# Kernel tuning notes

Measured on AMD Instinct MI355X. Metric: run time of the kernel, lower is better.

The kernel has to match this reference:

```python
import jax, jax.numpy as jnp
import numpy as np

TOP_K = 2
NUM_EXPERTS = 8

def setup_inputs() -> dict:
    key = jax.random.key(0)
    k_x, k_r, k_g, k_u, k_d = jax.random.split(key, 5)
    B, L, D, H, E = 1, 2048, 1024, 2048, NUM_EXPERTS
    scale = 0.02  # keep router logits / activations in a sane range
    return {
        "x": jax.random.normal(k_x, (B, L, D), dtype=jnp.float32),
        "router_w": jax.random.normal(k_r, (D, E), dtype=jnp.float32) * scale,
        "gate_w": jax.random.normal(k_g, (E, D, H), dtype=jnp.float32) * scale,
        "up_w": jax.random.normal(k_u, (E, D, H), dtype=jnp.float32) * scale,
        "down_w": jax.random.normal(k_d, (E, H, D), dtype=jnp.float32) * scale,
    }

def reference(x, router_w, gate_w, up_w, down_w):
    # x: (B, L, D)
    B, L, D = x.shape
    T = B * L
    E = router_w.shape[1]
    xf = x.reshape(T, D)

    # --- router: top-k softmax over selected logits (Mixtral-style) ---
    logits = xf @ router_w                      # (T, E)
    top_vals, top_idx = jax.lax.top_k(logits, TOP_K)  # (T, K)
    top_w = jax.nn.softmax(top_vals, axis=-1)   # (T, K)

    # combine weights scattered to dense (T, E); zeros for unrouted experts
    combine = jnp.zeros((T, E), dtype=x.dtype).at[
        jnp.arange(T)[:, None], top_idx
    ].add(top_w)

    # --- experts: SwiGLU, computed per expert, zero-weight tokens masked by combine ---
    gate = jnp.einsum('td,edh->eth', xf, gate_w)   # (E, T, H)
    up = jnp.einsum('td,edh->eth', xf, up_w)       # (E, T, H)
    hidden = jax.nn.silu(gate) * up                # (E, T, H)
    expert_out = jnp.einsum('eth,ehd->etd', hidden, down_w)  # (E, T, D)

    # --- weighted combine (equivalent to scatter_add over sorted assignments) ---
    y = jnp.einsum('etd,te->td', expert_out, combine)  # (T, D)
    return y.reshape(B, L, D)
```

## Files before the change

kernel.cpp:

```cpp
#include <hip/hip_runtime.h>
#include <hip/hip_bf16.h>
#include <stdint.h>

#define T_TOK 2048
#define DIM   1024
#define HDIM  2048
#define NE    8
#define ROWS_PAD 4224
#define TSLOTS 40

typedef __attribute__((ext_vector_type(8))) short bf16x8;
typedef __attribute__((ext_vector_type(4))) float f32x4;

__device__ __forceinline__ unsigned short f2bf(float f) {
    union { float f; unsigned int u; } v; v.f = f;
    unsigned int r = v.u + 0x7FFF + ((v.u >> 16) & 1);
    return (unsigned short)(r >> 16);
}

__device__ __forceinline__ float bf2f(unsigned short b) {
    union { unsigned int u; float f; } v; v.u = ((unsigned int)b) << 16;
    return v.f;
}

__device__ __forceinline__ void gload16(const void* g, void* l) {
    __builtin_amdgcn_global_load_lds(
        (const __attribute__((address_space(1))) void*)g,
        (__attribute__((address_space(3))) void*)l, 16, 0, 0);
}

#define NTT (3 * 16384)
__global__ void prep_kernel(const float* __restrict__ gw, const float* __restrict__ uw,
                            const float* __restrict__ dw,
                            unsigned short* __restrict__ WgT, unsigned short* __restrict__ WuT,
                            unsigned short* __restrict__ WdT,
                            const float* __restrict__ x, const float* __restrict__ rw,
                            int* __restrict__ counts, int* __restrict__ top_idx,
                            float* __restrict__ top_w) {
    __shared__ float tile[32][33];
    const int b = blockIdx.x;
    if (b < NTT) {
        const int m = b >> 14;
        const int t = b & 16383;
        const int e = t >> 11;
        const int rem = t & 2047;
        const float* in; unsigned short* out; int R, C, by, bx;
        if (m == 0)      { in = gw; out = WgT; R = DIM;  C = HDIM; by = rem >> 6; bx = rem & 63; }
        else if (m == 1) { in = uw; out = WuT; R = DIM;  C = HDIM; by = rem >> 6; bx = rem & 63; }
        else             { in = dw; out = WdT; R = HDIM; C = DIM;  by = rem >> 5; bx = rem & 31; }
        const float* ip = in + (size_t)e * R * C;
        unsigned short* op = out + (size_t)e * R * C;
        const int tx = threadIdx.x & 31, ty = threadIdx.x >> 5;
#pragma unroll
        for (int i = 0; i < 4; ++i)
            tile[ty + i * 8][tx] = ip[(size_t)(by * 32 + ty + i * 8) * C + bx * 32 + tx];
        __syncthreads();
#pragma unroll
        for (int i = 0; i < 2; ++i) {
            int oc = i * 16 + (threadIdx.x >> 4);
            int orw2 = (threadIdx.x & 15) * 2;
            ushort2 v;
            v.x = f2bf(tile[orw2][oc]);
            v.y = f2bf(tile[orw2 + 1][oc]);
            *(ushort2*)&op[(size_t)(bx * 32 + oc) * R + by * 32 + orw2] = v;
        }
    } else {
        const int wid = (b - NTT) * 4 + (threadIdx.x >> 6);
        const int lane = threadIdx.x & 63;
        if (wid >= T_TOK) return;
        float acc[NE];
#pragma unroll
        for (int e = 0; e < NE; ++e) acc[e] = 0.f;
        const float* xr = x + (size_t)wid * DIM;
        for (int i = lane; i < DIM; i += 64) {
            float xv = xr[i];
            const float* wr = rw + (size_t)i * NE;
#pragma unroll
            for (int e = 0; e < NE; ++e) acc[e] += xv * wr[e];
        }
#pragma unroll
        for (int off = 32; off; off >>= 1) {
#pragma unroll
            for (int e = 0; e < NE; ++e) acc[e] += __shfl_xor(acc[e], off, 64);
        }
        if (lane == 0) {
            float v0 = -1e30f, v1 = -1e30f; int i0 = 0, i1 = 0;
#pragma unroll
            for (int e = 0; e < NE; ++e) {
                float v = acc[e];
                if (v > v0) { v1 = v0; i1 = i0; v0 = v; i0 = e; }
                else if (v > v1) { v1 = v; i1 = e; }
            }
            float e1 = __expf(v1 - v0);
            float s = 1.f + e1;
            top_idx[wid * 2]     = i0;
            top_idx[wid * 2 + 1] = i1;
            top_w[wid * 2]     = 1.f / s;
            top_w[wid * 2 + 1] = e1 / s;
            atomicAdd(&counts[i0], 1);
            atomicAdd(&counts[i1], 1);
        }
    }
}

__global__ void scan_kernel(const int* __restrict__ counts, int* __restrict__ offsets,
                            int* __restrict__ cursors,
                            int* __restrict__ tl_e, int* __restrict__ tl_m) {
    if (threadIdx.x == 0) {
        int run = 0;
        for (int e = 0; e < NE; ++e) { offsets[e] = run; cursors[e] = run; run += counts[e]; }
        int n = 0;
        for (int e = 0; e < NE; ++e) {
            int mt = (counts[e] + 127) >> 7;
            for (int m = 0; m < mt && n < 64; ++m) { tl_e[n] = e; tl_m[n] = m; ++n; }
        }
        for (; n < 64; ++n) tl_e[n] = -1;
    }
}

__global__ void gather_kernel(const float* __restrict__ x, const int* __restrict__ top_idx,
                              const float* __restrict__ top_w, int* __restrict__ cursors,
                              int* __restrict__ row_tok, float* __restrict__ row_w,
                              unsigned short* __restrict__ Abuf) {
    int t = blockIdx.x;
    __shared__ int pos[2];
    if (threadIdx.x < 2) {
        int k = threadIdx.x;
        int e = top_idx[t * 2 + k];
        int p = atomicAdd(&cursors[e], 1);
        pos[k] = p;
        row_tok[p] = t;
        row_w[p] = top_w[t * 2 + k];
    }
    __syncthreads();
    const float4* xr = (const float4*)(x + (size_t)t * DIM);
    float4 v = xr[threadIdx.x];
    ushort4 b;
    b.x = f2bf(v.x); b.y = f2bf(v.y); b.z = f2bf(v.z); b.w = f2bf(v.w);
    ushort4* A4 = (ushort4*)Abuf;
    A4[(size_t)pos[0] * (DIM / 4) + threadIdx.x] = b;
    A4[(size_t)pos[1] * (DIM / 4) + threadIdx.x] = b;
}

__global__ __launch_bounds__(256, 2)
void gemm1_kernel(const unsigned short* __restrict__ Abuf,
                  const unsigned short* __restrict__ WgT,
                  const unsigned short* __restrict__ WuT,
                  unsigned short* __restrict__ Hbuf,
                  const int* __restrict__ offsets, const int* __restrict__ counts,
                  const int* __restrict__ tl_e, const int* __restrict__ tl_m) {
    const int slot = blockIdx.y;
    const int e = tl_e[slot];
    if (e < 0) return;
    const int mtile = tl_m[slot];
    const int cnt = counts[e];
    const int n0 = blockIdx.x * 64;
    const int row0 = offsets[e] + mtile * 128;

    __shared__ __align__(16) unsigned char lds_raw[65536];
    unsigned short* AsB = (unsigned short*)lds_raw;
    unsigned short* BgB = (unsigned short*)(lds_raw + 32768);
    unsigned short* BuB = (unsigned short*)(lds_raw + 49152);
    unsigned short* ex  = (unsigned short*)lds_raw;

    const int tid = threadIdx.x;
    const int lane = tid & 63;
    const int wave = tid >> 6;
    const int wm = wave >> 1;
    const int wu = wave & 1;

    f32x4 acc[4][4];
#pragma unroll
    for (int i = 0; i < 4; ++i)
#pragma unroll
        for (int j = 0; j < 4; ++j) acc[i][j] = (f32x4){0.f, 0.f, 0.f, 0.f};

    const int srow = tid >> 3;
    const int sc0 = tid & 7;
    const unsigned short* Aab = Abuf + (size_t)row0 * DIM;
    const unsigned short* Bgb = WgT + (size_t)e * HDIM * DIM + (size_t)n0 * DIM;
    const unsigned short* Bub = WuT + (size_t)e * HDIM * DIM + (size_t)n0 * DIM;

    auto stage = [&](int buf, int kt) {
#pragma unroll
        for (int i = 0; i < 4; ++i) {
            int row = i * 32 + srow;
            int csrc = sc0 ^ (row & 7);
            gload16(Aab + (size_t)row * DIM + kt + csrc * 8,
                    AsB + buf * 8192 + (i * 256 + tid) * 8);
        }
#pragma unroll
        for (int i = 0; i < 2; ++i) {
            int row = i * 32 + srow;
            int csrc = sc0 ^ (row & 7);
            size_t go = (size_t)row * DIM + kt + csrc * 8;
            gload16(Bgb + go, BgB + buf * 4096 + (i * 256 + tid) * 8);
            gload16(Bub + go, BuB + buf * 4096 + (i * 256 + tid) * 8);
        }
    };

    const int rsel = lane & 15;
    const int csrcf = lane >> 4;

    stage(0, 0);
    int cur = 0;
    for (int kt = 0; kt < DIM; kt += 64) {
        __syncthreads();
        if (kt + 64 < DIM) stage(cur ^ 1, kt + 64);
        const unsigned short* Ac = AsB + cur * 8192;
        const unsigned short* Bc = (wu ? BuB : BgB) + cur * 4096;
#pragma unroll
        for (int kk = 0; kk < 2; ++kk) {
            bf16x8 af[4], bb[4];
#pragma unroll
            for (int i = 0; i < 4; ++i) {
                int ra = wm * 64 + i * 16 + rsel;
                af[i] = *(const bf16x8*)&Ac[ra * 64 + ((kk * 4 + csrcf) ^ (ra & 7)) * 8];
                int rb = i * 16 + rsel;
                bb[i] = *(const bf16x8*)&Bc[rb * 64 + ((kk * 4 + csrcf) ^ (rb & 7)) * 8];
            }
#pragma unroll
            for (int i = 0; i < 4; ++i)
#pragma unroll
                for (int j = 0; j < 4; ++j)
                    acc[i][j] = __builtin_amdgcn_mfma_f32_16x16x32_bf16(af[i], bb[j], acc[i][j], 0, 0, 0);
        }
        cur ^= 1;
    }

    const int c = lane & 15, rbase = (lane >> 4) * 4;
    const int obase = offsets[e];
    __syncthreads();
    if (wu) {
#pragma unroll
        for (int i = 0; i < 4; ++i)
#pragma unroll
            for (int r = 0; r < 4; ++r) {
                int row64 = i * 16 + rbase + r;
#pragma unroll
                for (int j = 0; j < 4; ++j)
                    ex[wm * 4096 + row64 * 64 + j * 16 + c] = f2bf(acc[i][j][r]);
            }
    }
    __syncthreads();
    if (!wu) {
#pragma unroll
        for (int i = 0; i < 4; ++i) {
#pragma unroll
            for (int r = 0; r < 4; ++r) {
                int row64 = i * 16 + rbase + r;
                int lrow = mtile * 128 + wm * 64 + row64;
                if (lrow < cnt) {
                    size_t orow = (size_t)(obase + lrow);
#pragma unroll
                    for (int j = 0; j < 4; ++j) {
                        float g = acc[i][j][r];
                        float u = bf2f(ex[wm * 4096 + row64 * 64 + j * 16 + c]);
                        float h = g * u / (1.f + __expf(-g));
                        Hbuf[orow * HDIM + n0 + j * 16 + c] = f2bf(h);
                    }
                }
            }
        }
    }
}

__global__ __launch_bounds__(256, 2)
void gemm2_kernel(const unsigned short* __restrict__ Hbuf,
                  const unsigned short* __restrict__ WdT,
                  float* __restrict__ y,
                  const int* __restrict__ offsets, const int* __restrict__ counts,
                  const int* __restrict__ row_tok, const float* __restrict__ row_w,
                  const int* __restrict__ tl_e, const int* __restrict__ tl_m) {
    const int slot = blockIdx.y;
    const int e = tl_e[slot];
    if (e < 0) return;
    const int mtile = tl_m[slot];
    const int kc = blockIdx.z;
    const int cnt = counts[e];
    const int n0 = blockIdx.x * 128;
    const int row0 = offsets[e] + mtile * 128;

    __shared__ unsigned short As[2][128 * 64];
    __shared__ unsigned short Bs[2][128 * 64];

    const int tid = threadIdx.x;
    const int lane = tid & 63;
    const int wave = tid >> 6;
    const int wm = wave >> 1, wn = wave & 1;

    f32x4 acc[4][4];
#pragma unroll
    for (int i = 0; i < 4; ++i)
#pragma unroll
        for (int j = 0; j < 4; ++j) acc[i][j] = (f32x4){0.f, 0.f, 0.f, 0.f};

    const int srow0 = tid >> 3;
    const int sc0 = tid & 7;
    const unsigned short* Aab = Hbuf + (size_t)row0 * HDIM;
    const unsigned short* Bbb = WdT + (size_t)e * DIM * HDIM + (size_t)n0 * HDIM;

    auto stage = [&](int buf, int kt) {
#pragma unroll
        for (int i = 0; i < 4; ++i) {
            int row = i * 32 + srow0;
            int csrc = sc0 ^ (row & 7);
            size_t go = (size_t)row * HDIM + kt + csrc * 8;
            int lo = (i * 256 + tid) * 8;
            gload16(Aab + go, &As[buf][lo]);
            gload16(Bbb + go, &Bs[buf][lo]);
        }
    };

    const int rsel = lane & 15;
    const int csrcf = lane >> 4;

    const int kbeg = kc * (HDIM / 2);
    const int kend = kbeg + (HDIM / 2);

    stage(0, kbeg);
    int cur = 0;
    for (int kt = kbeg; kt < kend; kt += 64) {
        __syncthreads();
        if (kt + 64 < kend) stage(cur ^ 1, kt + 64);
        const unsigned short* Ac = As[cur];
        const unsigned short* Bc = Bs[cur];
#pragma unroll
        for (int kk = 0; kk < 2; ++kk) {
            bf16x8 af[4], bf[4];
#pragma unroll
            for (int i = 0; i < 4; ++i) {
                int ra = wm * 64 + i * 16 + rsel;
                af[i] = *(const bf16x8*)&Ac[ra * 64 + ((kk * 4 + csrcf) ^ (ra & 7)) * 8];
                int rb = wn * 64 + i * 16 + rsel;
                bf[i] = *(const bf16x8*)&Bc[rb * 64 + ((kk * 4 + csrcf) ^ (rb & 7)) * 8];
            }
#pragma unroll
            for (int i = 0; i < 4; ++i)
#pragma unroll
                for (int j = 0; j < 4; ++j)
                    acc[i][j] = __builtin_amdgcn_mfma_f32_16x16x32_bf16(af[i], bf[j], acc[i][j], 0, 0, 0);
        }
        cur ^= 1;
    }

    const int c = lane & 15, rbase = (lane >> 4) * 4;
    const int obase = offsets[e];
#pragma unroll
    for (int i = 0; i < 4; ++i) {
#pragma unroll
        for (int r = 0; r < 4; ++r) {
            int lrow = mtile * 128 + wm * 64 + i * 16 + rbase + r;
            if (lrow < cnt) {
                int grow = obase + lrow;
                int tok = row_tok[grow];
                float w = row_w[grow];
#pragma unroll
                for (int j = 0; j < 4; ++j) {
                    atomicAdd(&y[(size_t)tok * DIM + n0 + wn * 64 + j * 16 + c], w * acc[i][j][r]);
                }
            }
        }
    }
}

extern "C" void kernel_launch(void* const* d_in, const int* in_sizes, int n_in,
                              void* d_out, int out_size, void* d_ws, size_t ws_size,
                              hipStream_t stream) {
    const float* x  = (const float*)d_in[0];
    const float* rw = (const float*)d_in[1];
    const float* gw = (const float*)d_in[2];
    const float* uw = (const float*)d_in[3];
    const float* dw = (const float*)d_in[4];
    float* y = (float*)d_out;

    char* ws = (char*)d_ws;
    int*   counts  = (int*)(ws + 0);
    int*   cursors = (int*)(ws + 32);
    int*   offsets = (int*)(ws + 64);
    int*   top_idx = (int*)(ws + 128);
    float* top_w   = (float*)(ws + 128 + 16384);
    int*   row_tok = (int*)(ws + 128 + 32768);
    float* row_w   = (float*)(ws + 128 + 32768 + 16896);
    int*   tl_e    = (int*)(ws + 128 + 32768 + 2 * 16896);
    int*   tl_m    = (int*)(ws + 128 + 32768 + 2 * 16896 + 256);
    size_t off = 128 + 32768 + 2 * 16896 + 512;
    off = (off + 255) & ~(size_t)255;
    unsigned short* Abuf = (unsigned short*)(ws + off); off += (size_t)ROWS_PAD * DIM * 2;
    unsigned short* Hbuf = (unsigned short*)(ws + off); off += (size_t)ROWS_PAD * HDIM * 2;
    unsigned short* WgT  = (unsigned short*)(ws + off); off += (size_t)NE * DIM * HDIM * 2;
    unsigned short* WuT  = (unsigned short*)(ws + off); off += (size_t)NE * DIM * HDIM * 2;
    unsigned short* WdT  = (unsigned short*)(ws + off); off += (size_t)NE * DIM * HDIM * 2;
    if (ws_size < off) return;

    hipMemsetAsync(counts, 0, 32, stream);
    hipMemsetAsync(d_out, 0, (size_t)out_size * 4, stream);

    prep_kernel<<<NTT + T_TOK / 4, 256, 0, stream>>>(gw, uw, dw, WgT, WuT, WdT,
                                                     x, rw, counts, top_idx, top_w);
    scan_kernel<<<1, 64, 0, stream>>>(counts, offsets, cursors, tl_e, tl_m);
    gather_kernel<<<T_TOK, 256, 0, stream>>>(x, top_idx, top_w, cursors, row_tok, row_w, Abuf);

    gemm1_kernel<<<dim3(HDIM / 64, TSLOTS), 256, 0, stream>>>(Abuf, WgT, WuT, Hbuf,
                                                              offsets, counts, tl_e, tl_m);
    gemm2_kernel<<<dim3(DIM / 128, TSLOTS, 2), 256, 0, stream>>>(Hbuf, WdT, y, offsets, counts,
                                                                 row_tok, row_w, tl_e, tl_m);
}
```

Before: 262.7 us.

## Fuse fp32 weight transpose and bf16 conversion into GEMM B-tile staging

```diff
diff --git a/kernel.cpp b/kernel.cpp
--- a/kernel.cpp
+++ b/kernel.cpp
@@ -10,6 +10,7 @@
 #define TSLOTS 40
 
 typedef __attribute__((ext_vector_type(8))) short bf16x8;
+typedef __attribute__((ext_vector_type(8))) unsigned short u16x8;
 typedef __attribute__((ext_vector_type(4))) float f32x4;
 
 __device__ __forceinline__ unsigned short f2bf(float f) {
@@ -29,77 +30,43 @@
         (__attribute__((address_space(3))) void*)l, 16, 0, 0);
 }
 
-#define NTT (3 * 16384)
-__global__ void prep_kernel(const float* __restrict__ gw, const float* __restrict__ uw,
-                            const float* __restrict__ dw,
-                            unsigned short* __restrict__ WgT, unsigned short* __restrict__ WuT,
-                            unsigned short* __restrict__ WdT,
-                            const float* __restrict__ x, const float* __restrict__ rw,
-                            int* __restrict__ counts, int* __restrict__ top_idx,
-                            float* __restrict__ top_w) {
-    __shared__ float tile[32][33];
-    const int b = blockIdx.x;
-    if (b < NTT) {
-        const int m = b >> 14;
-        const int t = b & 16383;
-        const int e = t >> 11;
-        const int rem = t & 2047;
-        const float* in; unsigned short* out; int R, C, by, bx;
-        if (m == 0)      { in = gw; out = WgT; R = DIM;  C = HDIM; by = rem >> 6; bx = rem & 63; }
-        else if (m == 1) { in = uw; out = WuT; R = DIM;  C = HDIM; by = rem >> 6; bx = rem & 63; }
-        else             { in = dw; out = WdT; R = HDIM; C = DIM;  by = rem >> 5; bx = rem & 31; }
-        const float* ip = in + (size_t)e * R * C;
-        unsigned short* op = out + (size_t)e * R * C;
-        const int tx = threadIdx.x & 31, ty = threadIdx.x >> 5;
-#pragma unroll
-        for (int i = 0; i < 4; ++i)
-            tile[ty + i * 8][tx] = ip[(size_t)(by * 32 + ty + i * 8) * C + bx * 32 + tx];
-        __syncthreads();
-#pragma unroll
-        for (int i = 0; i < 2; ++i) {
-            int oc = i * 16 + (threadIdx.x >> 4);
-            int orw2 = (threadIdx.x & 15) * 2;
-            ushort2 v;
-            v.x = f2bf(tile[orw2][oc]);
-            v.y = f2bf(tile[orw2 + 1][oc]);
-            *(ushort2*)&op[(size_t)(bx * 32 + oc) * R + by * 32 + orw2] = v;
-        }
-    } else {
-        const int wid = (b - NTT) * 4 + (threadIdx.x >> 6);
-        const int lane = threadIdx.x & 63;
-        if (wid >= T_TOK) return;
-        float acc[NE];
-#pragma unroll
-        for (int e = 0; e < NE; ++e) acc[e] = 0.f;
-        const float* xr = x + (size_t)wid * DIM;
-        for (int i = lane; i < DIM; i += 64) {
-            float xv = xr[i];
-            const float* wr = rw + (size_t)i * NE;
-#pragma unroll
-            for (int e = 0; e < NE; ++e) acc[e] += xv * wr[e];
-        }
-#pragma unroll
-        for (int off = 32; off; off >>= 1) {
-#pragma unroll
-            for (int e = 0; e < NE; ++e) acc[e] += __shfl_xor(acc[e], off, 64);
-        }
-        if (lane == 0) {
-            float v0 = -1e30f, v1 = -1e30f; int i0 = 0, i1 = 0;
-#pragma unroll
-            for (int e = 0; e < NE; ++e) {
-                float v = acc[e];
-                if (v > v0) { v1 = v0; i1 = i0; v0 = v; i0 = e; }
-                else if (v > v1) { v1 = v; i1 = e; }
-            }
-            float e1 = __expf(v1 - v0);
-            float s = 1.f + e1;
-            top_idx[wid * 2]     = i0;
-            top_idx[wid * 2 + 1] = i1;
-            top_w[wid * 2]     = 1.f / s;
-            top_w[wid * 2 + 1] = e1 / s;
-            atomicAdd(&counts[i0], 1);
-            atomicAdd(&counts[i1], 1);
-        }
+__global__ void router_kernel(const float* __restrict__ x, const float* __restrict__ rw,
+                              int* __restrict__ counts, int* __restrict__ top_idx,
+                              float* __restrict__ top_w) {
+    int wid = (blockIdx.x * blockDim.x + threadIdx.x) >> 6;
+    int lane = threadIdx.x & 63;
+    if (wid >= T_TOK) return;
+    float acc[NE];
+#pragma unroll
+    for (int e = 0; e < NE; ++e) acc[e] = 0.f;
+    const float* xr = x + (size_t)wid * DIM;
+    for (int i = lane; i < DIM; i += 64) {
+        float xv = xr[i];
+        const float* wr = rw + (size_t)i * NE;
+#pragma unroll
+        for (int e = 0; e < NE; ++e) acc[e] += xv * wr[e];
+    }
+#pragma unroll
+    for (int off = 32; off; off >>= 1) {
+#pragma unroll
+        for (int e = 0; e < NE; ++e) acc[e] += __shfl_xor(acc[e], off, 64);
+    }
+    if (lane == 0) {
+        float v0 = -1e30f, v1 = -1e30f; int i0 = 0, i1 = 0;
+#pragma unroll
+        for (int e = 0; e < NE; ++e) {
+            float v = acc[e];
+            if (v > v0) { v1 = v0; i1 = i0; v0 = v; i0 = e; }
+            else if (v > v1) { v1 = v; i1 = e; }
+        }
+        float e1 = __expf(v1 - v0);
+        float s = 1.f + e1;
+        top_idx[wid * 2]     = i0;
+        top_idx[wid * 2 + 1] = i1;
+        top_w[wid * 2]     = 1.f / s;
+        top_w[wid * 2 + 1] = e1 / s;
+        atomicAdd(&counts[i0], 1);
+        atomicAdd(&counts[i1], 1);
     }
 }
 
@@ -144,8 +111,8 @@
 
 __global__ __launch_bounds__(256, 2)
 void gemm1_kernel(const unsigned short* __restrict__ Abuf,
-                  const unsigned short* __restrict__ WgT,
-                  const unsigned short* __restrict__ WuT,
+                  const float* __restrict__ gw,
+                  const float* __restrict__ uw,
                   unsigned short* __restrict__ Hbuf,
                   const int* __restrict__ offsets, const int* __restrict__ counts,
                   const int* __restrict__ tl_e, const int* __restrict__ tl_m) {
@@ -178,10 +145,8 @@
     const int srow = tid >> 3;
     const int sc0 = tid & 7;
     const unsigned short* Aab = Abuf + (size_t)row0 * DIM;
-    const unsigned short* Bgb = WgT + (size_t)e * HDIM * DIM + (size_t)n0 * DIM;
-    const unsigned short* Bub = WuT + (size_t)e * HDIM * DIM + (size_t)n0 * DIM;
-
-    auto stage = [&](int buf, int kt) {
+
+    auto stageA = [&](int buf, int kt) {
 #pragma unroll
         for (int i = 0; i < 4; ++i) {
             int row = i * 32 + srow;
@@ -189,24 +154,54 @@
             gload16(Aab + (size_t)row * DIM + kt + csrc * 8,
                     AsB + buf * 8192 + (i * 256 + tid) * 8);
         }
-#pragma unroll
-        for (int i = 0; i < 2; ++i) {
-            int row = i * 32 + srow;
-            int csrc = sc0 ^ (row & 7);
-            size_t go = (size_t)row * DIM + kt + csrc * 8;
-            gload16(Bgb + go, BgB + buf * 4096 + (i * 256 + tid) * 8);
-            gload16(Bub + go, BuB + buf * 4096 + (i * 256 + tid) * 8);
+    };
+
+    const int bn = tid & 63;
+    const int bc0 = tid >> 6;
+    const float* Bgb = gw + (size_t)e * DIM * HDIM + n0 + bn;
+    const float* Bub = uw + (size_t)e * DIM * HDIM + n0 + bn;
+
+    float bgl[2][8], bul[2][8];
+    auto bload = [&](int kt) {
+#pragma unroll
+        for (int cc = 0; cc < 2; ++cc) {
+            int c = bc0 + cc * 4;
+            const float* gs = Bgb + (size_t)(kt + c * 8) * HDIM;
+            const float* us = Bub + (size_t)(kt + c * 8) * HDIM;
+#pragma unroll
+            for (int jj = 0; jj < 8; ++jj) {
+                bgl[cc][jj] = gs[(size_t)jj * HDIM];
+                bul[cc][jj] = us[(size_t)jj * HDIM];
+            }
+        }
+    };
+    auto bwrite = [&](int buf) {
+#pragma unroll
+        for (int cc = 0; cc < 2; ++cc) {
+            int c = bc0 + cc * 4;
+            int la = bn * 64 + ((c ^ (bn & 7)) * 8);
+            u16x8 vg, vu;
+#pragma unroll
+            for (int jj = 0; jj < 8; ++jj) {
+                vg[jj] = f2bf(bgl[cc][jj]);
+                vu[jj] = f2bf(bul[cc][jj]);
+            }
+            *(u16x8*)&BgB[buf * 4096 + la] = vg;
+            *(u16x8*)&BuB[buf * 4096 + la] = vu;
         }
     };
 
     const int rsel = lane & 15;
     const int csrcf = lane >> 4;
 
-    stage(0, 0);
+    stageA(0, 0);
+    bload(0);
+    bwrite(0);
     int cur = 0;
     for (int kt = 0; kt < DIM; kt += 64) {
         __syncthreads();
-        if (kt + 64 < DIM) stage(cur ^ 1, kt + 64);
+        const bool pre = (kt + 64 < DIM);
+        if (pre) { stageA(cur ^ 1, kt + 64); bload(kt + 64); }
         const unsigned short* Ac = AsB + cur * 8192;
         const unsigned short* Bc = (wu ? BuB : BgB) + cur * 4096;
 #pragma unroll
@@ -225,6 +220,7 @@
                 for (int j = 0; j < 4; ++j)
                     acc[i][j] = __builtin_amdgcn_mfma_f32_16x16x32_bf16(af[i], bb[j], acc[i][j], 0, 0, 0);
         }
+        if (pre) bwrite(cur ^ 1);
         cur ^= 1;
     }
 
@@ -267,7 +263,7 @@
 
 __global__ __launch_bounds__(256, 2)
 void gemm2_kernel(const unsigned short* __restrict__ Hbuf,
-                  const unsigned short* __restrict__ WdT,
+                  const float* __restrict__ dw,
                   float* __restrict__ y,
                   const int* __restrict__ offsets, const int* __restrict__ counts,
                   const int* __restrict__ row_tok, const float* __restrict__ row_w,
@@ -298,17 +294,40 @@
     const int srow0 = tid >> 3;
     const int sc0 = tid & 7;
     const unsigned short* Aab = Hbuf + (size_t)row0 * HDIM;
-    const unsigned short* Bbb = WdT + (size_t)e * DIM * HDIM + (size_t)n0 * HDIM;
-
-    auto stage = [&](int buf, int kt) {
+
+    auto stageA = [&](int buf, int kt) {
 #pragma unroll
         for (int i = 0; i < 4; ++i) {
             int row = i * 32 + srow0;
             int csrc = sc0 ^ (row & 7);
-            size_t go = (size_t)row * HDIM + kt + csrc * 8;
-            int lo = (i * 256 + tid) * 8;
-            gload16(Aab + go, &As[buf][lo]);
-            gload16(Bbb + go, &Bs[buf][lo]);
+            gload16(Aab + (size_t)row * HDIM + kt + csrc * 8,
+                    &As[buf][(i * 256 + tid) * 8]);
+        }
+    };
+
+    const int bn = tid & 127;
+    const int bc0 = (tid >> 7) * 4;
+    const float* Bbb = dw + (size_t)e * HDIM * DIM + n0 + bn;
+
+    float bl[4][8];
+    auto bload = [&](int kt) {
+#pragma unroll
+        for (int cc = 0; cc < 4; ++cc) {
+            const float* bs = Bbb + (size_t)(kt + (bc0 + cc) * 8) * DIM;
+#pragma unroll
+            for (int jj = 0; jj < 8; ++jj)
+                bl[cc][jj] = bs[(size_t)jj * DIM];
+        }
+    };
+    auto bwrite = [&](int buf) {
+#pragma unroll
+        for (int cc = 0; cc < 4; ++cc) {
+            int c = bc0 + cc;
+            int la = bn * 64 + ((c ^ (bn & 7)) * 8);
+            u16x8 v;
+#pragma unroll
+            for (int jj = 0; jj < 8; ++jj) v[jj] = f2bf(bl[cc][jj]);
+            *(u16x8*)&Bs[buf][la] = v;
         }
     };
 
@@ -318,11 +337,14 @@
     const int kbeg = kc * (HDIM / 2);
     const int kend = kbeg + (HDIM / 2);
 
-    stage(0, kbeg);
+    stageA(0, kbeg);
+    bload(kbeg);
+    bwrite(0);
     int cur = 0;
     for (int kt = kbeg; kt < kend; kt += 64) {
         __syncthreads();
-        if (kt + 64 < kend) stage(cur ^ 1, kt + 64);
+        const bool pre = (kt + 64 < kend);
+        if (pre) { stageA(cur ^ 1, kt + 64); bload(kt + 64); }
         const unsigned short* Ac = As[cur];
         const unsigned short* Bc = Bs[cur];
 #pragma unroll
@@ -341,6 +363,7 @@
                 for (int j = 0; j < 4; ++j)
                     acc[i][j] = __builtin_amdgcn_mfma_f32_16x16x32_bf16(af[i], bf[j], acc[i][j], 0, 0, 0);
         }
+        if (pre) bwrite(cur ^ 1);
         cur ^= 1;
     }
 
@@ -388,21 +411,17 @@
     off = (off + 255) & ~(size_t)255;
     unsigned short* Abuf = (unsigned short*)(ws + off); off += (size_t)ROWS_PAD * DIM * 2;
     unsigned short* Hbuf = (unsigned short*)(ws + off); off += (size_t)ROWS_PAD * HDIM * 2;
-    unsigned short* WgT  = (unsigned short*)(ws + off); off += (size_t)NE * DIM * HDIM * 2;
-    unsigned short* WuT  = (unsigned short*)(ws + off); off += (size_t)NE * DIM * HDIM * 2;
-    unsigned short* WdT  = (unsigned short*)(ws + off); off += (size_t)NE * DIM * HDIM * 2;
     if (ws_size < off) return;
 
     hipMemsetAsync(counts, 0, 32, stream);
     hipMemsetAsync(d_out, 0, (size_t)out_size * 4, stream);
 
-    prep_kernel<<<NTT + T_TOK / 4, 256, 0, stream>>>(gw, uw, dw, WgT, WuT, WdT,
-                                                     x, rw, counts, top_idx, top_w);
+    router_kernel<<<T_TOK / 4, 256, 0, stream>>>(x, rw, counts, top_idx, top_w);
     scan_kernel<<<1, 64, 0, stream>>>(counts, offsets, cursors, tl_e, tl_m);
     gather_kernel<<<T_TOK, 256, 0, stream>>>(x, top_idx, top_w, cursors, row_tok, row_w, Abuf);
 
-    gemm1_kernel<<<dim3(HDIM / 64, TSLOTS), 256, 0, stream>>>(Abuf, WgT, WuT, Hbuf,
+    gemm1_kernel<<<dim3(HDIM / 64, TSLOTS), 256, 0, stream>>>(Abuf, gw, uw, Hbuf,
                                                               offsets, counts, tl_e, tl_m);
-    gemm2_kernel<<<dim3(DIM / 128, TSLOTS, 2), 256, 0, stream>>>(Hbuf, WdT, y, offsets, counts,
+    gemm2_kernel<<<dim3(DIM / 128, TSLOTS, 2), 256, 0, stream>>>(Hbuf, dw, y, offsets, counts,
                                                                  row_tok, row_w, tl_e, tl_m);
 }
```

Result: faster. 249.1 us (-5.2%).
